# Performance work log

Hardware: AMD Instinct MI355X
Metric: run time of the kernel (lower is better)

Reference implementation:

```python
import jax, jax.numpy as jnp
import numpy as np

N, E = 25000, 400000
NF, EF, HNF, HEF = 32, 32, 128, 128
NOUT, EOUT = 32, 32
D_N, D_E = HNF + NF, HEF + EF  # concat dims fed to the GNN layer


def _glorot(key, shape):
    return jax.random.normal(key, shape, jnp.float32) / np.sqrt(shape[0])


def setup_inputs() -> dict:
    key = jax.random.key(0)
    ks = jax.random.split(key, 10)
    return {
        "nf": jax.random.normal(ks[0], (N, NF), jnp.float32),
        "ef": jax.random.normal(ks[1], (E, EF), jnp.float32),
        "src": jax.random.randint(ks[2], (E,), 0, N),
        "dst": jax.random.randint(ks[3], (E,), 0, N),
        # AttnMPNNLayer params: edge model, attention logit model, node model
        "W_edge": _glorot(ks[4], (2 * D_N + D_E, HEF)),
        "b_edge": jnp.zeros((HEF,), jnp.float32),
        "W_attn": _glorot(ks[5], (2 * D_N + D_E, 1)),
        "b_attn": jnp.zeros((1,), jnp.float32),
        "W_node": _glorot(ks[6], (D_N + HEF, HNF)),
        "b_node": jnp.zeros((HNF,), jnp.float32),
        # output heads (MLP with num_neurons=[] -> single Linear)
        "W_nout": _glorot(ks[7], (HNF, NOUT)),
        "b_nout": jnp.zeros((NOUT,), jnp.float32),
        "W_eout": _glorot(ks[8], (HEF, EOUT)),
        "b_eout": jnp.zeros((EOUT,), jnp.float32),
        "n_iters": 3,
    }


def _attn_mpnn_layer(hnf, hef, src, dst, W_edge, b_edge, W_attn, b_attn, W_node, b_node):
    """Attention message passing: gather endpoints, edge MLP + attn logit,
    edge-softmax over incoming edges (per dst node), scatter-aggregate, node MLP."""
    n = hnf.shape[0]
    e_in = jnp.concatenate([hnf[src], hnf[dst], hef], axis=-1)   # [E, 2*D_N + D_E]
    m = jax.nn.relu(e_in @ W_edge + b_edge)                      # [E, HEF] new edge feats
    logit = (e_in @ W_attn + b_attn)[:, 0]                       # [E]
    # numerically stable edge softmax grouped by destination node
    lmax = jax.ops.segment_max(logit, dst, num_segments=n)
    lmax = jnp.where(jnp.isfinite(lmax), lmax, 0.0)              # isolated nodes -> 0
    a = jnp.exp(logit - lmax[dst])
    denom = jax.ops.segment_sum(a, dst, num_segments=n)
    alpha = a / jnp.maximum(denom[dst], 1e-16)
    agg = jax.ops.segment_sum(alpha[:, None] * m, dst, num_segments=n)  # [N, HEF]
    un = jax.nn.relu(jnp.concatenate([hnf, agg], axis=-1) @ W_node + b_node)  # [N, HNF]
    return un, m


def reference(nf, ef, src, dst, W_edge, b_edge, W_attn, b_attn, W_node, b_node,
              W_nout, b_nout, W_eout, b_eout, n_iters):
    hnf = jnp.zeros((nf.shape[0], HNF), nf.dtype)
    hef = jnp.zeros((ef.shape[0], HEF), ef.dtype)
    for _ in range(n_iters):
        hnf = jnp.concatenate([hnf, nf], axis=-1)   # input re-injection
        hef = jnp.concatenate([hef, ef], axis=-1)
        hnf, hef = _attn_mpnn_layer(hnf, hef, src, dst,
                                    W_edge, b_edge, W_attn, b_attn, W_node, b_node)
    unf = hnf @ W_nout + b_nout
    uef = hef @ W_eout + b_eout
    return unf, uef
```

## Files before the change

kernel.cpp:

```cpp
#include <hip/hip_runtime.h>


#define GN 25000
#define GE 400000
#define NODE_BLKS 196
#define EDGE_BLKS 6250
#define HEAD_EBLKS 3125

typedef unsigned short u16;
typedef __attribute__((ext_vector_type(8))) short bf16x8;
typedef __attribute__((ext_vector_type(4))) float f32x4;

__device__ inline float b2f(u16 v) {
  union { unsigned int u; float f; } x; x.u = ((unsigned int)v) << 16; return x.f;
}
__device__ inline u16 f2b(float f) {
  union { float f; unsigned int u; } x; x.f = f;
  unsigned int u = x.u;
  u += 0x7fffu + ((u >> 16) & 1u);
  return (u16)(u >> 16);
}

__global__ void detect_dtype(const void* nf, int* flag) {
  if (blockIdx.x == 0 && threadIdx.x == 0) {
    const u16* p = (const u16*)nf;
    int cnt = 0;
    for (int i = 0; i < 512; i += 2) {
      int e = (p[i] >> 7) & 0xFF;
      if (e >= 0x70 && e <= 0x85) cnt++;
    }
    *flag = (cnt < 128) ? 1 : 0;
  }
}

__global__ void convert_kernel(const void* src, u16* dst, long n, const int* flag) {
  int f32 = *flag;
  long i = (long)blockIdx.x * blockDim.x + threadIdx.x;
  long stride = (long)gridDim.x * blockDim.x;
  for (; i < n; i += stride)
    dst[i] = f32 ? f2b(((const float*)src)[i]) : ((const u16*)src)[i];
}

__global__ void gather_ef(const void* ef, const int* eid, u16* efc, const int* flag) {
  int f32 = *flag;
  long idx = (long)blockIdx.x * blockDim.x + threadIdx.x;
  long stride = (long)gridDim.x * blockDim.x;
  long ntot = (long)GE * 32;
  for (; idx < ntot; idx += stride) {
    long j = idx >> 5;
    int c = (int)(idx & 31);
    long e = eid[j];
    efc[idx] = f32 ? f2b(((const float*)ef)[e * 32 + c]) : ((const u16*)ef)[e * 32 + c];
  }
}

__global__ void prep_weights(const void* We, const void* Wn, const void* Wa,
                             const void* Won, const void* Woe,
                             const void* be, const void* ba, const void* bn,
                             const void* bno, const void* beo,
                             u16* WeT, u16* WnpT, u16* WnuT, u16* WoN, u16* WoE,
                             u16* Wac, u16* bec, u16* bac, u16* bnc, u16* bnoc, u16* beoc,
                             const int* flag) {
  int f32 = *flag;
  auto ld = [&](const void* p, long i) -> u16 {
    return f32 ? f2b(((const float*)p)[i]) : ((const u16*)p)[i];
  };
  int tid = blockIdx.x * blockDim.x + threadIdx.x;
  int nt = gridDim.x * blockDim.x;
  for (int i = tid; i < 128 * 160; i += nt) { int n = i / 160, k = i % 160; WeT[i] = ld(We, (long)(320 + k) * 128 + n); }
  for (int i = tid; i < 256 * 160; i += nt) {
    int c = i / 160, k = i % 160;
    WnpT[i] = (c < 128) ? ld(We, (long)k * 128 + c) : ld(We, (long)(160 + k) * 128 + (c - 128));
  }
  for (int i = tid; i < 128 * 288; i += nt) { int c = i / 288, k = i % 288; WnuT[i] = ld(Wn, (long)k * 128 + c); }
  for (int i = tid; i < 32 * 128; i += nt) {
    int c = i / 128, k = i % 128;
    WoN[i] = ld(Won, (long)k * 32 + c);
    WoE[i] = ld(Woe, (long)k * 32 + c);
  }
  for (int i = tid; i < 480; i += nt) Wac[i] = ld(Wa, i);
  for (int i = tid; i < 128; i += nt) { bec[i] = ld(be, i); bnc[i] = ld(bn, i); }
  for (int i = tid; i < 32; i += nt) { bnoc[i] = ld(bno, i); beoc[i] = ld(beo, i); }
  if (tid == 0) bac[0] = ld(ba, 0);
}

__global__ void hist_kernel(const int* dst, int* counts, int n) {
  for (int e = blockIdx.x * blockDim.x + threadIdx.x; e < n; e += gridDim.x * blockDim.x)
    atomicAdd(&counts[dst[e]], 1);
}

__global__ __launch_bounds__(256) void scan_kernel(int* cursor, int* rowptr, int n) {
  __shared__ int part[256];
  int t = threadIdx.x;
  int per = (n + 255) / 256;
  int lo = t * per;
  int hi = lo + per; if (hi > n) hi = n;
  if (lo > n) lo = n;
  int s = 0;
  for (int i = lo; i < hi; ++i) s += cursor[i];
  part[t] = s;
  __syncthreads();
  for (int off = 1; off < 256; off <<= 1) {
    int v = (t >= off) ? part[t - off] : 0;
    __syncthreads();
    part[t] += v;
    __syncthreads();
  }
  int run = (t > 0) ? part[t - 1] : 0;
  for (int i = lo; i < hi; ++i) {
    int c = cursor[i];
    cursor[i] = run;
    rowptr[i + 1] = run + c;
    run += c;
  }
  if (t == 0) rowptr[0] = 0;
}

__global__ void fill_kernel(const int* src, const int* dst, int* cursor, int* eid,
                            int* srcs, int* dsts, int n) {
  for (int e = blockIdx.x * blockDim.x + threadIdx.x; e < n; e += gridDim.x * blockDim.x) {
    int d = dst[e];
    int p = atomicAdd(&cursor[d], 1);
    eid[p] = e;
    srcs[p] = src[e];
    dsts[p] = d;
  }
}

__global__ __launch_bounds__(256)
void node_proj(const u16* HNF, const u16* nf, const u16* WnpT, const u16* W_attn,
               u16* Xs, u16* Xd, float* as_, float* ad_, int kc0, int nrows) {
  __shared__ union {
    struct { __align__(16) u16 A[128][40]; __align__(16) u16 B[128][40]; } st;
    u16 C[128][130];
  } sm;
  __shared__ float dotbuf[128][2];
  int sel = blockIdx.y, blk = blockIdx.x, tid = threadIdx.x;
  int lane = tid & 63, wv = tid >> 6, wr = wv & 1, wc = wv >> 1;
  const u16* BT = WnpT + sel * 128 * 160;
  u16* OUT = sel ? Xd : Xs;
  float* AOUT = sel ? ad_ : as_;
  const u16* wa = W_attn + sel * 160;
  f32x4 acc[4][4];
  f32x4 zf = {0.f, 0.f, 0.f, 0.f};
  for (int i = 0; i < 4; ++i) for (int j = 0; j < 4; ++j) acc[i][j] = zf;
  float dp = 0.f;
  int arow = tid >> 1, ahalf = (tid & 1) * 16;
  int r0 = blk * 128;
  for (int kc = kc0; kc < 5; ++kc) {
    {
      int r = r0 + arow;
      uint4 v0 = make_uint4(0, 0, 0, 0), v1 = make_uint4(0, 0, 0, 0);
      if (r < nrows) {
        const uint4* p = (kc < 4) ? (const uint4*)(HNF + (size_t)r * 128 + kc * 32 + ahalf)
                                  : (const uint4*)(nf + (size_t)r * 32 + ahalf);
        v0 = p[0]; v1 = p[1];
      }
      *(uint4*)&sm.st.A[arow][ahalf] = v0;
      *(uint4*)&sm.st.A[arow][ahalf + 8] = v1;
    }
    {
      const uint4* p = (const uint4*)(BT + arow * 160 + kc * 32 + ahalf);
      uint4 v0 = p[0], v1 = p[1];
      *(uint4*)&sm.st.B[arow][ahalf] = v0;
      *(uint4*)&sm.st.B[arow][ahalf + 8] = v1;
    }
    __syncthreads();
    {
      float s = 0.f;
      for (int j = 0; j < 16; ++j) s += b2f(sm.st.A[arow][ahalf + j]) * b2f(wa[kc * 32 + ahalf + j]);
      dp += s;
    }
    int q = lane >> 4, l16 = lane & 15;
    bf16x8 af[4], bfr[4];
    for (int i = 0; i < 4; ++i) af[i] = *(const bf16x8*)&sm.st.A[wr * 64 + i * 16 + l16][q * 8];
    for (int j = 0; j < 4; ++j) bfr[j] = *(const bf16x8*)&sm.st.B[wc * 64 + j * 16 + l16][q * 8];
    for (int i = 0; i < 4; ++i)
      for (int j = 0; j < 4; ++j)
        acc[i][j] = __builtin_amdgcn_mfma_f32_16x16x32_bf16(af[i], bfr[j], acc[i][j], 0, 0, 0);
    __syncthreads();
  }
  dotbuf[arow][tid & 1] = dp;
  {
    int q = lane >> 4, l16 = lane & 15;
    for (int i = 0; i < 4; ++i)
      for (int j = 0; j < 4; ++j) {
        int col = wc * 64 + j * 16 + l16;
        for (int rr = 0; rr < 4; ++rr) {
          int row = wr * 64 + i * 16 + q * 4 + rr;
          sm.C[row][col] = f2b(acc[i][j][rr]);
        }
      }
  }
  __syncthreads();
  if (tid < 128) {
    int r = r0 + tid;
    if (r < nrows) AOUT[r] = dotbuf[tid][0] + dotbuf[tid][1];
  }
  {
    int r = tid >> 1, h = (tid & 1) * 64;
    int rg = r0 + r;
    if (rg < nrows) {
      uint4* po = (uint4*)(OUT + (size_t)rg * 128 + h);
      for (int k = 0; k < 8; ++k) {
        unsigned int a0 = *(const unsigned int*)&sm.C[r][h + k * 8];
        unsigned int a1 = *(const unsigned int*)&sm.C[r][h + k * 8 + 2];
        unsigned int a2 = *(const unsigned int*)&sm.C[r][h + k * 8 + 4];
        unsigned int a3 = *(const unsigned int*)&sm.C[r][h + k * 8 + 6];
        po[k] = make_uint4(a0, a1, a2, a3);
      }
    }
  }
}

__global__ __launch_bounds__(256, 4)
void edge_fused(u16* HEF, const u16* ef, const u16* WeT, const u16* W_attn,
                const u16* b_edge, const u16* b_attn, const int* srcs, const int* dsts,
                const u16* Xs, const u16* Xd, const float* as_, const float* ad_,
                float* logit, int kc0) {
  __shared__ union {
    struct { __align__(16) u16 A[64][40]; __align__(16) u16 B[128][40]; } st;
    float C[64][65];
  } sm;
  __shared__ float dotbuf[64];
  int blk = blockIdx.x, tid = threadIdx.x;
  int lane = tid & 63, wv = tid >> 6, wr = wv & 1, wc = wv >> 1;
  int q = lane >> 4, l16 = lane & 15;
  f32x4 acc[2][4];
  f32x4 zf = {0.f, 0.f, 0.f, 0.f};
  for (int i = 0; i < 2; ++i) for (int j = 0; j < 4; ++j) acc[i][j] = zf;
  float dp[2] = {0.f, 0.f};
  long e0 = (long)blk * 64;
  long ea = e0 + (tid >> 2);
  int qp = (tid & 3) * 8;
  int brow = tid >> 1, bh = (tid & 1) * 16;
  const u16* wa = W_attn + 320;
  uint4 va, vb0, vb1;
  {
    const uint4* pa = (kc0 < 4) ? (const uint4*)(HEF + ea * 128 + kc0 * 32 + qp)
                                : (const uint4*)(ef + ea * 32 + qp);
    va = pa[0];
    const uint4* pb = (const uint4*)(WeT + brow * 160 + kc0 * 32 + bh);
    vb0 = pb[0]; vb1 = pb[1];
  }
  for (int kc = kc0; kc < 5; ++kc) {
    *(uint4*)&sm.st.A[tid >> 2][qp] = va;
    *(uint4*)&sm.st.B[brow][bh] = vb0;
    *(uint4*)&sm.st.B[brow][bh + 8] = vb1;
    __syncthreads();
    if (kc < 4) {
      int kn = kc + 1;
      const uint4* pa = (kn < 4) ? (const uint4*)(HEF + ea * 128 + kn * 32 + qp)
                                 : (const uint4*)(ef + ea * 32 + qp);
      va = pa[0];
      const uint4* pb = (const uint4*)(WeT + brow * 160 + kn * 32 + bh);
      vb0 = pb[0]; vb1 = pb[1];
    }
    bf16x8 af[2], bfr[4];
    for (int i = 0; i < 2; ++i) af[i] = *(const bf16x8*)&sm.st.A[wr * 32 + i * 16 + l16][q * 8];
    for (int j = 0; j < 4; ++j) bfr[j] = *(const bf16x8*)&sm.st.B[wc * 64 + j * 16 + l16][q * 8];
    if (wc == 0) {
      bf16x8 wv8 = *(const bf16x8*)&wa[kc * 32 + q * 8];
      float wf[8];
      for (int j = 0; j < 8; ++j) wf[j] = b2f((u16)wv8[j]);
      for (int i = 0; i < 2; ++i)
        for (int j = 0; j < 8; ++j) dp[i] += b2f((u16)af[i][j]) * wf[j];
    }
    for (int i = 0; i < 2; ++i)
      for (int j = 0; j < 4; ++j)
        acc[i][j] = __builtin_amdgcn_mfma_f32_16x16x32_bf16(af[i], bfr[j], acc[i][j], 0, 0, 0);
    __syncthreads();
  }
  if (wc == 0) {
    for (int i = 0; i < 2; ++i) {
      dp[i] += __shfl_xor(dp[i], 16);
      dp[i] += __shfl_xor(dp[i], 32);
    }
    if (q == 0)
      for (int i = 0; i < 2; ++i) dotbuf[wr * 32 + i * 16 + l16] = dp[i];
  }
  int r = tid >> 2, qh = tid & 3;
  long e = e0 + r;
  int s = srcs[e], d = dsts[e];
  for (int p = 0; p < 2; ++p) {
    int cb = p * 64 + qh * 16;
    const uint4* ps = (const uint4*)(Xs + (size_t)s * 128 + cb);
    const uint4* pd = (const uint4*)(Xd + (size_t)d * 128 + cb);
    uint4 gs0 = ps[0], gs1 = ps[1], gd0 = pd[0], gd1 = pd[1];
    if (p) __syncthreads();
    if (wc == p) {
      for (int i = 0; i < 2; ++i)
        for (int j = 0; j < 4; ++j) {
          int col = j * 16 + l16;
          float bb = b2f(b_edge[p * 64 + col]);
          for (int rr = 0; rr < 4; ++rr)
            sm.C[wr * 32 + i * 16 + q * 4 + rr][col] = acc[i][j][rr] + bb;
        }
    }
    __syncthreads();
    if (p == 0 && tid < 64) {
      long ee = e0 + tid;
      logit[ee] = dotbuf[tid] + as_[srcs[ee]] + ad_[dsts[ee]] + b2f(b_attn[0]);
    }
    unsigned int us[8], ud[8];
    *(uint4*)&us[0] = gs0; *(uint4*)&us[4] = gs1;
    *(uint4*)&ud[0] = gd0; *(uint4*)&ud[4] = gd1;
    unsigned int ov[8];
    for (int w = 0; w < 8; ++w) {
      float c0 = sm.C[r][qh * 16 + 2 * w];
      float c1 = sm.C[r][qh * 16 + 2 * w + 1];
      float v0 = c0 + b2f((u16)(us[w] & 0xffffu)) + b2f((u16)(ud[w] & 0xffffu));
      float v1 = c1 + b2f((u16)(us[w] >> 16)) + b2f((u16)(ud[w] >> 16));
      ov[w] = (unsigned int)f2b(fmaxf(v0, 0.f)) | ((unsigned int)f2b(fmaxf(v1, 0.f)) << 16);
    }
    uint4* po = (uint4*)(HEF + e * 128 + cb);
    po[0] = *(uint4*)&ov[0];
    po[1] = *(uint4*)&ov[4];
  }
}

__global__ __launch_bounds__(256)
void aggregate(const int* rowptr, const float* logit, const u16* M, u16* AGG, int nrows) {
  int gw = (blockIdx.x * blockDim.x + threadIdx.x) >> 6;
  int lane = threadIdx.x & 63;
  if (gw >= nrows) return;
  int beg = rowptr[gw], end = rowptr[gw + 1];
  int sub = lane >> 4, cl = lane & 15;
  float mx = -1e30f;
  for (int j = beg + lane; j < end; j += 64) mx = fmaxf(mx, logit[j]);
  for (int off = 32; off > 0; off >>= 1) mx = fmaxf(mx, __shfl_xor(mx, off));
  float acc[8] = {0.f, 0.f, 0.f, 0.f, 0.f, 0.f, 0.f, 0.f};
  float denom = 0.f;
  for (int j0 = beg; j0 < end; j0 += 4) {
    int j = j0 + sub;
    float w = 0.f;
    uint4 mv = make_uint4(0, 0, 0, 0);
    if (j < end) {
      w = __expf(logit[j] - mx);
      mv = *(const uint4*)(M + (size_t)j * 128 + cl * 8);
    }
    denom += w;
    const unsigned int* mw = (const unsigned int*)&mv;
    for (int t = 0; t < 4; ++t) {
      acc[2 * t]     += w * b2f((u16)(mw[t] & 0xffffu));
      acc[2 * t + 1] += w * b2f((u16)(mw[t] >> 16));
    }
  }
  denom += __shfl_xor(denom, 16);
  denom += __shfl_xor(denom, 32);
  for (int t = 0; t < 8; ++t) {
    acc[t] += __shfl_xor(acc[t], 16);
    acc[t] += __shfl_xor(acc[t], 32);
  }
  float inv = 1.0f / fmaxf(denom, 1e-16f);
  if (sub == 0) {
    unsigned int ov[4];
    for (int t = 0; t < 4; ++t)
      ov[t] = (unsigned int)f2b(acc[2 * t] * inv) | ((unsigned int)f2b(acc[2 * t + 1] * inv) << 16);
    *(uint4*)(AGG + (size_t)gw * 128 + cl * 8) = *(uint4*)ov;
  }
}

__global__ __launch_bounds__(256)
void node_update(u16* HNF, const u16* nf, const u16* AGG, const u16* WnuT,
                 const u16* b_node, int kc0, int nrows) {
  __shared__ union {
    struct { __align__(16) u16 A[128][40]; __align__(16) u16 B[128][40]; } st;
    u16 C[128][130];
  } sm;
  int blk = blockIdx.x, tid = threadIdx.x;
  int lane = tid & 63, wv = tid >> 6, wr = wv & 1, wc = wv >> 1;
  f32x4 acc[4][4];
  f32x4 zf = {0.f, 0.f, 0.f, 0.f};
  for (int i = 0; i < 4; ++i) for (int j = 0; j < 4; ++j) acc[i][j] = zf;
  int arow = tid >> 1, ahalf = (tid & 1) * 16;
  int r0 = blk * 128;
  for (int kc = kc0; kc < 9; ++kc) {
    {
      int r = r0 + arow;
      uint4 v0 = make_uint4(0, 0, 0, 0), v1 = make_uint4(0, 0, 0, 0);
      if (r < nrows) {
        const u16* p;
        if (kc < 4) p = HNF + (size_t)r * 128 + kc * 32 + ahalf;
        else if (kc == 4) p = nf + (size_t)r * 32 + ahalf;
        else p = AGG + (size_t)r * 128 + (kc - 5) * 32 + ahalf;
        v0 = ((const uint4*)p)[0];
        v1 = ((const uint4*)p)[1];
      }
      *(uint4*)&sm.st.A[arow][ahalf] = v0;
      *(uint4*)&sm.st.A[arow][ahalf + 8] = v1;
    }
    {
      const uint4* p = (const uint4*)(WnuT + arow * 288 + kc * 32 + ahalf);
      uint4 v0 = p[0], v1 = p[1];
      *(uint4*)&sm.st.B[arow][ahalf] = v0;
      *(uint4*)&sm.st.B[arow][ahalf + 8] = v1;
    }
    __syncthreads();
    int q = lane >> 4, l16 = lane & 15;
    bf16x8 af[4], bfr[4];
    for (int i = 0; i < 4; ++i) af[i] = *(const bf16x8*)&sm.st.A[wr * 64 + i * 16 + l16][q * 8];
    for (int j = 0; j < 4; ++j) bfr[j] = *(const bf16x8*)&sm.st.B[wc * 64 + j * 16 + l16][q * 8];
    for (int i = 0; i < 4; ++i)
      for (int j = 0; j < 4; ++j)
        acc[i][j] = __builtin_amdgcn_mfma_f32_16x16x32_bf16(af[i], bfr[j], acc[i][j], 0, 0, 0);
    __syncthreads();
  }
  int q = lane >> 4, l16 = lane & 15;
  for (int i = 0; i < 4; ++i)
    for (int j = 0; j < 4; ++j) {
      int col = wc * 64 + j * 16 + l16;
      float bb = b2f(b_node[col]);
      for (int rr = 0; rr < 4; ++rr) {
        int row = wr * 64 + i * 16 + q * 4 + rr;
        sm.C[row][col] = f2b(fmaxf(acc[i][j][rr] + bb, 0.f));
      }
    }
  __syncthreads();
  {
    int r = tid >> 1, h = (tid & 1) * 64;
    int rg = r0 + r;
    if (rg < nrows) {
      uint4* po = (uint4*)(HNF + (size_t)rg * 128 + h);
      for (int k = 0; k < 8; ++k) {
        unsigned int a0 = *(const unsigned int*)&sm.C[r][h + k * 8];
        unsigned int a1 = *(const unsigned int*)&sm.C[r][h + k * 8 + 2];
        unsigned int a2 = *(const unsigned int*)&sm.C[r][h + k * 8 + 4];
        unsigned int a3 = *(const unsigned int*)&sm.C[r][h + k * 8 + 6];
        po[k] = make_uint4(a0, a1, a2, a3);
      }
    }
  }
}

__global__ __launch_bounds__(256)
void head_kernel(const u16* IN, const u16* WT, const u16* bias, float* OUT, long R,
                 const int* remap) {
  __shared__ __align__(16) u16 Asm[128][40];
  __shared__ __align__(16) u16 Bsm[32][40];
  int blk = blockIdx.x, tid = threadIdx.x;
  int lane = tid & 63, wv = tid >> 6;
  f32x4 acc[2][2];
  f32x4 zf = {0.f, 0.f, 0.f, 0.f};
  for (int i = 0; i < 2; ++i) for (int j = 0; j < 2; ++j) acc[i][j] = zf;
  int arow = tid >> 1, ahalf = (tid & 1) * 16;
  long r0 = (long)blk * 128;
  for (int kc = 0; kc < 4; ++kc) {
    {
      long r = r0 + arow;
      uint4 v0 = make_uint4(0, 0, 0, 0), v1 = make_uint4(0, 0, 0, 0);
      if (r < R) {
        const uint4* p = (const uint4*)(IN + r * 128 + kc * 32 + ahalf);
        v0 = p[0]; v1 = p[1];
      }
      *(uint4*)&Asm[arow][ahalf] = v0;
      *(uint4*)&Asm[arow][ahalf + 8] = v1;
    }
    if (tid < 64) {
      const uint4* p = (const uint4*)(WT + arow * 128 + kc * 32 + ahalf);
      uint4 v0 = p[0], v1 = p[1];
      *(uint4*)&Bsm[arow][ahalf] = v0;
      *(uint4*)&Bsm[arow][ahalf + 8] = v1;
    }
    __syncthreads();
    int q = lane >> 4, l16 = lane & 15;
    bf16x8 af[2], bfr[2];
    for (int i = 0; i < 2; ++i) af[i] = *(const bf16x8*)&Asm[wv * 32 + i * 16 + l16][q * 8];
    for (int j = 0; j < 2; ++j) bfr[j] = *(const bf16x8*)&Bsm[j * 16 + l16][q * 8];
    for (int i = 0; i < 2; ++i)
      for (int j = 0; j < 2; ++j)
        acc[i][j] = __builtin_amdgcn_mfma_f32_16x16x32_bf16(af[i], bfr[j], acc[i][j], 0, 0, 0);
    __syncthreads();
  }
  int q = lane >> 4, l16 = lane & 15;
  for (int i = 0; i < 2; ++i)
    for (int rr = 0; rr < 4; ++rr) {
      long r = r0 + wv * 32 + i * 16 + q * 4 + rr;
      if (r < R) {
        long ro = remap ? (long)remap[r] : r;
        for (int j = 0; j < 2; ++j) {
          int col = j * 16 + l16;
          OUT[ro * 32 + col] = acc[i][j][rr] + b2f(bias[col]);
        }
      }
    }
}

extern "C" void kernel_launch(void* const* d_in, const int* in_sizes, int n_in,
                              void* d_out, int out_size, void* d_ws, size_t ws_size,
                              hipStream_t stream) {
  const size_t REQUIRED = 160000000;
  if (ws_size < REQUIRED) return;

  const void* nf_r = d_in[0];
  const void* ef_r = d_in[1];
  const int* src = (const int*)d_in[2];
  const int* dst = (const int*)d_in[3];

  char* ws = (char*)d_ws;
  auto alloc = [&](size_t bytes) {
    char* p = ws;
    ws += (bytes + 255) & ~(size_t)255;
    return p;
  };
  u16* HEF = (u16*)alloc((size_t)GE * 128 * 2);
  u16* HNF = (u16*)alloc((size_t)GN * 128 * 2);
  u16* Xs = (u16*)alloc((size_t)GN * 128 * 2);
  u16* Xd = (u16*)alloc((size_t)GN * 128 * 2);
  float* as_ = (float*)alloc((size_t)GN * 4);
  float* ad_ = (float*)alloc((size_t)GN * 4);
  float* logit = (float*)alloc((size_t)GE * 4);
  int* rowptr = (int*)alloc((size_t)(GN + 1) * 4);
  int* cursor = (int*)alloc((size_t)GN * 4);
  int* eid = (int*)alloc((size_t)GE * 4);
  int* srcs = (int*)alloc((size_t)GE * 4);
  int* dsts = (int*)alloc((size_t)GE * 4);
  u16* WeT = (u16*)alloc(128 * 160 * 2);
  u16* WnpT = (u16*)alloc(256 * 160 * 2);
  u16* WnuT = (u16*)alloc(128 * 288 * 2);
  u16* WoN = (u16*)alloc(32 * 128 * 2);
  u16* WoE = (u16*)alloc(32 * 128 * 2);
  u16* nfc = (u16*)alloc((size_t)GN * 32 * 2);
  u16* efc = (u16*)alloc((size_t)GE * 32 * 2);
  u16* bec = (u16*)alloc(128 * 2);
  u16* Wac = (u16*)alloc(480 * 2);
  u16* bac = (u16*)alloc(2);
  u16* bnc = (u16*)alloc(128 * 2);
  u16* bnoc = (u16*)alloc(32 * 2);
  u16* beoc = (u16*)alloc(32 * 2);
  int* dflag = (int*)alloc(4);
  u16* AGG = Xs;

  detect_dtype<<<1, 64, 0, stream>>>(nf_r, dflag);
  hipMemsetAsync(cursor, 0, (size_t)GN * 4, stream);
  hist_kernel<<<1563, 256, 0, stream>>>(dst, cursor, GE);
  scan_kernel<<<1, 256, 0, stream>>>(cursor, rowptr, GN);
  fill_kernel<<<1563, 256, 0, stream>>>(src, dst, cursor, eid, srcs, dsts, GE);

  convert_kernel<<<784, 256, 0, stream>>>(nf_r, nfc, (long)GN * 32, dflag);
  gather_ef<<<6250, 256, 0, stream>>>(ef_r, eid, efc, dflag);
  prep_weights<<<128, 256, 0, stream>>>(d_in[4], d_in[8], d_in[6], d_in[10], d_in[12],
                                        d_in[5], d_in[7], d_in[9], d_in[11], d_in[13],
                                        WeT, WnpT, WnuT, WoN, WoE,
                                        Wac, bec, bac, bnc, bnoc, beoc, dflag);

  for (int iter = 0; iter < 3; ++iter) {
    int kc0 = (iter == 0) ? 4 : 0;
    dim3 npgrid(NODE_BLKS, 2);
    node_proj<<<npgrid, 256, 0, stream>>>(HNF, nfc, WnpT, Wac, Xs, Xd, as_, ad_, kc0, GN);
    edge_fused<<<EDGE_BLKS, 256, 0, stream>>>(HEF, efc, WeT, Wac, bec, bac, srcs, dsts,
                                              Xs, Xd, as_, ad_, logit, kc0);
    aggregate<<<(GN + 3) / 4, 256, 0, stream>>>(rowptr, logit, HEF, AGG, GN);
    node_update<<<NODE_BLKS, 256, 0, stream>>>(HNF, nfc, AGG, WnuT, bnc, kc0, GN);
  }

  float* out_nf = (float*)d_out;
  float* out_ef = (float*)d_out + (size_t)GN * 32;
  head_kernel<<<NODE_BLKS, 256, 0, stream>>>(HNF, WoN, bnoc, out_nf, GN, nullptr);
  head_kernel<<<HEAD_EBLKS, 256, 0, stream>>>(HEF, WoE, beoc, out_ef, GE, eid);
}
```

Measured before the change: 641.7 us.

## Template edge kernel on start chunk, double-buffer A tile, load weights to registers

The edge kernel is templated on the starting K chunk so its loop fully unrolls. All activation chunks are prefetched into registers up front, and the A tile is double-buffered in shared memory, which drops one barrier per chunk. The weight B fragments are read straight from global into registers instead of being staged through LDS. The aggregate kernel now has each lane handle 16 columns, with 8 edges processed per step instead of 4. These changes trade higher register pressure, and possibly lower occupancy, for fewer barriers and more memory parallelism.

New measurement: 708.5 us. 10.4% more time.

```diff
diff --git a/kernel.cpp b/kernel.cpp
--- a/kernel.cpp
+++ b/kernel.cpp
@@ -213,13 +213,14 @@
   }
 }
 
+template <int KC0>
 __global__ __launch_bounds__(256, 4)
 void edge_fused(u16* HEF, const u16* ef, const u16* WeT, const u16* W_attn,
                 const u16* b_edge, const u16* b_attn, const int* srcs, const int* dsts,
                 const u16* Xs, const u16* Xd, const float* as_, const float* ad_,
-                float* logit, int kc0) {
+                float* logit) {
   __shared__ union {
-    struct { __align__(16) u16 A[64][40]; __align__(16) u16 B[128][40]; } st;
+    __align__(16) u16 A[2][64][40];
     float C[64][65];
   } sm;
   __shared__ float dotbuf[64];
@@ -233,32 +234,30 @@
   long e0 = (long)blk * 64;
   long ea = e0 + (tid >> 2);
   int qp = (tid & 3) * 8;
-  int brow = tid >> 1, bh = (tid & 1) * 16;
   const u16* wa = W_attn + 320;
-  uint4 va, vb0, vb1;
-  {
-    const uint4* pa = (kc0 < 4) ? (const uint4*)(HEF + ea * 128 + kc0 * 32 + qp)
-                                : (const uint4*)(ef + ea * 32 + qp);
-    va = pa[0];
-    const uint4* pb = (const uint4*)(WeT + brow * 160 + kc0 * 32 + bh);
-    vb0 = pb[0]; vb1 = pb[1];
-  }
-  for (int kc = kc0; kc < 5; ++kc) {
-    *(uint4*)&sm.st.A[tid >> 2][qp] = va;
-    *(uint4*)&sm.st.B[brow][bh] = vb0;
-    *(uint4*)&sm.st.B[brow][bh + 8] = vb1;
-    __syncthreads();
+
+  uint4 va[5];
+#pragma unroll
+  for (int kc = KC0; kc < 5; ++kc)
+    va[kc] = (kc < 4) ? *(const uint4*)(HEF + ea * 128 + kc * 32 + qp)
+                      : *(const uint4*)(ef + ea * 32 + qp);
+  bf16x8 bf[5][4];
+#pragma unroll
+  for (int j = 0; j < 4; ++j)
+    bf[KC0][j] = *(const bf16x8*)(WeT + (size_t)(wc * 64 + j * 16 + l16) * 160 + KC0 * 32 + q * 8);
+
+#pragma unroll
+  for (int kc = KC0; kc < 5; ++kc) {
+    int buf = kc & 1;
+    *(uint4*)&sm.A[buf][tid >> 2][qp] = va[kc];
     if (kc < 4) {
-      int kn = kc + 1;
-      const uint4* pa = (kn < 4) ? (const uint4*)(HEF + ea * 128 + kn * 32 + qp)
-                                 : (const uint4*)(ef + ea * 32 + qp);
-      va = pa[0];
-      const uint4* pb = (const uint4*)(WeT + brow * 160 + kn * 32 + bh);
-      vb0 = pb[0]; vb1 = pb[1];
-    }
-    bf16x8 af[2], bfr[4];
-    for (int i = 0; i < 2; ++i) af[i] = *(const bf16x8*)&sm.st.A[wr * 32 + i * 16 + l16][q * 8];
-    for (int j = 0; j < 4; ++j) bfr[j] = *(const bf16x8*)&sm.st.B[wc * 64 + j * 16 + l16][q * 8];
+#pragma unroll
+      for (int j = 0; j < 4; ++j)
+        bf[kc + 1][j] = *(const bf16x8*)(WeT + (size_t)(wc * 64 + j * 16 + l16) * 160 + (kc + 1) * 32 + q * 8);
+    }
+    __syncthreads();
+    bf16x8 af[2];
+    for (int i = 0; i < 2; ++i) af[i] = *(const bf16x8*)&sm.A[buf][wr * 32 + i * 16 + l16][q * 8];
     if (wc == 0) {
       bf16x8 wv8 = *(const bf16x8*)&wa[kc * 32 + q * 8];
       float wf[8];
@@ -268,8 +267,7 @@
     }
     for (int i = 0; i < 2; ++i)
       for (int j = 0; j < 4; ++j)
-        acc[i][j] = __builtin_amdgcn_mfma_f32_16x16x32_bf16(af[i], bfr[j], acc[i][j], 0, 0, 0);
-    __syncthreads();
+        acc[i][j] = __builtin_amdgcn_mfma_f32_16x16x32_bf16(af[i], bf[kc][j], acc[i][j], 0, 0, 0);
   }
   if (wc == 0) {
     for (int i = 0; i < 2; ++i) {
@@ -282,12 +280,13 @@
   int r = tid >> 2, qh = tid & 3;
   long e = e0 + r;
   int s = srcs[e], d = dsts[e];
+#pragma unroll
   for (int p = 0; p < 2; ++p) {
     int cb = p * 64 + qh * 16;
     const uint4* ps = (const uint4*)(Xs + (size_t)s * 128 + cb);
     const uint4* pd = (const uint4*)(Xd + (size_t)d * 128 + cb);
     uint4 gs0 = ps[0], gs1 = ps[1], gd0 = pd[0], gd1 = pd[1];
-    if (p) __syncthreads();
+    __syncthreads();
     if (wc == p) {
       for (int i = 0; i < 2; ++i)
         for (int j = 0; j < 4; ++j) {
@@ -325,39 +324,48 @@
   int lane = threadIdx.x & 63;
   if (gw >= nrows) return;
   int beg = rowptr[gw], end = rowptr[gw + 1];
-  int sub = lane >> 4, cl = lane & 15;
+  int sub = lane >> 3, cl = lane & 7;
   float mx = -1e30f;
   for (int j = beg + lane; j < end; j += 64) mx = fmaxf(mx, logit[j]);
   for (int off = 32; off > 0; off >>= 1) mx = fmaxf(mx, __shfl_xor(mx, off));
-  float acc[8] = {0.f, 0.f, 0.f, 0.f, 0.f, 0.f, 0.f, 0.f};
+  float acc[16];
+  for (int t = 0; t < 16; ++t) acc[t] = 0.f;
   float denom = 0.f;
-  for (int j0 = beg; j0 < end; j0 += 4) {
+  for (int j0 = beg; j0 < end; j0 += 8) {
     int j = j0 + sub;
     float w = 0.f;
-    uint4 mv = make_uint4(0, 0, 0, 0);
+    uint4 m0 = make_uint4(0, 0, 0, 0), m1 = make_uint4(0, 0, 0, 0);
     if (j < end) {
       w = __expf(logit[j] - mx);
-      mv = *(const uint4*)(M + (size_t)j * 128 + cl * 8);
+      const uint4* mp = (const uint4*)(M + (size_t)j * 128 + cl * 16);
+      m0 = mp[0]; m1 = mp[1];
     }
     denom += w;
-    const unsigned int* mw = (const unsigned int*)&mv;
+    const unsigned int* mw0 = (const unsigned int*)&m0;
+    const unsigned int* mw1 = (const unsigned int*)&m1;
     for (int t = 0; t < 4; ++t) {
-      acc[2 * t]     += w * b2f((u16)(mw[t] & 0xffffu));
-      acc[2 * t + 1] += w * b2f((u16)(mw[t] >> 16));
-    }
-  }
+      acc[2 * t]     += w * b2f((u16)(mw0[t] & 0xffffu));
+      acc[2 * t + 1] += w * b2f((u16)(mw0[t] >> 16));
+      acc[8 + 2 * t]     += w * b2f((u16)(mw1[t] & 0xffffu));
+      acc[8 + 2 * t + 1] += w * b2f((u16)(mw1[t] >> 16));
+    }
+  }
+  denom += __shfl_xor(denom, 8);
   denom += __shfl_xor(denom, 16);
   denom += __shfl_xor(denom, 32);
-  for (int t = 0; t < 8; ++t) {
+  for (int t = 0; t < 16; ++t) {
+    acc[t] += __shfl_xor(acc[t], 8);
     acc[t] += __shfl_xor(acc[t], 16);
     acc[t] += __shfl_xor(acc[t], 32);
   }
   float inv = 1.0f / fmaxf(denom, 1e-16f);
   if (sub == 0) {
-    unsigned int ov[4];
-    for (int t = 0; t < 4; ++t)
+    unsigned int ov[8];
+    for (int t = 0; t < 8; ++t)
       ov[t] = (unsigned int)f2b(acc[2 * t] * inv) | ((unsigned int)f2b(acc[2 * t + 1] * inv) << 16);
-    *(uint4*)(AGG + (size_t)gw * 128 + cl * 8) = *(uint4*)ov;
+    uint4* po = (uint4*)(AGG + (size_t)gw * 128 + cl * 16);
+    po[0] = *(uint4*)&ov[0];
+    po[1] = *(uint4*)&ov[4];
   }
 }
 
@@ -548,8 +556,12 @@
     int kc0 = (iter == 0) ? 4 : 0;
     dim3 npgrid(NODE_BLKS, 2);
     node_proj<<<npgrid, 256, 0, stream>>>(HNF, nfc, WnpT, Wac, Xs, Xd, as_, ad_, kc0, GN);
-    edge_fused<<<EDGE_BLKS, 256, 0, stream>>>(HEF, efc, WeT, Wac, bec, bac, srcs, dsts,
-                                              Xs, Xd, as_, ad_, logit, kc0);
+    if (iter == 0)
+      edge_fused<4><<<EDGE_BLKS, 256, 0, stream>>>(HEF, efc, WeT, Wac, bec, bac, srcs, dsts,
+                                                   Xs, Xd, as_, ad_, logit);
+    else
+      edge_fused<0><<<EDGE_BLKS, 256, 0, stream>>>(HEF, efc, WeT, Wac, bec, bac, srcs, dsts,
+                                                   Xs, Xd, as_, ad_, logit);
     aggregate<<<(GN + 3) / 4, 256, 0, stream>>>(rowptr, logit, HEF, AGG, GN);
     node_update<<<NODE_BLKS, 256, 0, stream>>>(HNF, nfc, AGG, WnuT, bnc, kc0, GN);
   }
```
